# Kernel tuning notes

Measured on AMD Instinct MI355X. Metric: run time of the kernel, lower is better.

The kernel has to match this reference:

```python
import jax, jax.numpy as jnp
import numpy as np

N_NODES = 100000
N_EDGES = 1000000
D_FEAT = 64
N_FILTER = 64
N_CLASSES = 16


def gcn_norm(edge_idx, n):
    """Add self-loops and compute symmetric normalization D^-1/2 (A+I) D^-1/2."""
    loop = jnp.arange(n, dtype=edge_idx.dtype)
    src = jnp.concatenate([edge_idx[0], loop])  # [E+N]
    dst = jnp.concatenate([edge_idx[1], loop])  # [E+N]
    w = jnp.ones(src.shape[0], dtype=jnp.float32)
    deg = jax.ops.segment_sum(w, dst, num_segments=n)  # in-degree incl. self-loop
    dinv = jnp.where(deg > 0, jax.lax.rsqrt(deg), 0.0)
    norm = dinv[src] * w * dinv[dst]  # [E+N]
    return src, dst, norm


def gcn_conv(x, W, b, src, dst, norm, n):
    h = x @ W                                   # [n, f] dense transform first (f <= d)
    msg = h[src] * norm[:, None]                # gather + scale  [E+N, f]
    out = jax.ops.segment_sum(msg, dst, num_segments=n)  # scatter-add  [n, f]
    return out + b


def setup_inputs() -> dict:
    key = jax.random.key(0)
    k1, k2, k3, k4 = jax.random.split(key, 4)
    X = jax.random.normal(k1, (N_NODES, D_FEAT), dtype=jnp.float32)
    edge_idx = jax.random.randint(k2, (2, N_EDGES), 0, N_NODES, dtype=jnp.int64)
    W1 = jax.random.normal(k3, (D_FEAT, N_FILTER), dtype=jnp.float32) * 0.05
    b1 = jnp.zeros((N_FILTER,), dtype=jnp.float32)
    W2 = jax.random.normal(k4, (N_FILTER, N_CLASSES), dtype=jnp.float32) * 0.05
    b2 = jnp.zeros((N_CLASSES,), dtype=jnp.float32)
    return {"X": X, "edge_idx": edge_idx, "W1": W1, "b1": b1, "W2": W2, "b2": b2}


def reference(X, edge_idx, W1, b1, W2, b2):
    n = X.shape[0]
    src, dst, norm = gcn_norm(edge_idx, n)
    x = gcn_conv(X, W1, b1, src, dst, norm, n)
    x = jax.nn.relu(x)
    # dropout p=0 -> identity
    x = gcn_conv(x, W2, b2, src, dst, norm, n)
    return x  # raw logits; pred_layer is not applied in the torch forward
```

## Files before the change

kernel.cpp:

```cpp
#include <hip/hip_runtime.h>
#include <hip/hip_bf16.h>


constexpr int N = 100000;
constexpr int E = 1000000;
constexpr int NB = (N + 511) / 512;
constexpr int CAP = 6144;
constexpr int CSTRIDE = 32;
constexpr int CHUNK = 2048;
constexpr int NBLK = (E + CHUNK - 1) / CHUNK;
constexpr int BT = 512;
constexpr int NPW = 4;
constexpr int NW = (N + NPW - 1) / NPW;
constexpr int NWBLK = (NW + 3) / 4;

__device__ __forceinline__ float bflo(unsigned u) { return __uint_as_float(u << 16); }
__device__ __forceinline__ float bfhi(unsigned u) { return __uint_as_float(u & 0xffff0000u); }

__device__ __forceinline__ void wait_lgkm0() {
    __builtin_amdgcn_s_waitcnt(0xc07f);
    __builtin_amdgcn_sched_barrier(0);
}

__global__ void k_bfill(const int* __restrict__ src, const int* __restrict__ dst,
                        int* __restrict__ cursor, int* __restrict__ bkt) {
    __shared__ int hist[256];
    __shared__ int lbase[256];
    __shared__ int gbase[256];
    __shared__ int lcur[256];
    __shared__ int ws[8];
    __shared__ int stage[CHUNK];
    __shared__ unsigned char sbkt[CHUNK];
    int t = threadIdx.x;
    int lane = t & 63;
    int e0 = blockIdx.x * CHUNK;
    int cnt = min(CHUNK, E - e0);

    if (t < 256) hist[t] = 0;
    __syncthreads();
    for (int j = t; j < cnt; j += BT)
        atomicAdd(&hist[dst[e0 + j] >> 9], 1);
    __syncthreads();
    int h = (t < 256) ? hist[t] : 0;
    int v = h;
#pragma unroll
    for (int off = 1; off < 64; off <<= 1) {
        int u = __shfl_up(v, off);
        if (lane >= off) v += u;
    }
    if (lane == 63) ws[t >> 6] = v;
    __syncthreads();
    int add = 0;
    for (int i = 0; i < (t >> 6); ++i) add += ws[i];
    int inc = v + add;
    if (t < 256) { lbase[t] = inc - h; lcur[t] = 0; }
    if (t < NB) gbase[t] = h ? atomicAdd(&cursor[t * CSTRIDE], h) : 0;
    __syncthreads();
    for (int j = t; j < cnt; j += BT) {
        int d = dst[e0 + j];
        int b = d >> 9;
        int pos = lbase[b] + atomicAdd(&lcur[b], 1);
        stage[pos] = ((d & 511) << 17) | src[e0 + j];
        sbkt[pos] = (unsigned char)b;
    }
    __syncthreads();
    for (int j = t; j < cnt; j += BT) {
        int b = sbkt[j];
        int gpos = gbase[b] + (j - lbase[b]);
        if (gpos < CAP) bkt[b * CAP + gpos] = stage[j];
    }
}

__global__ void k_bfine(const int* __restrict__ cursor, const int* __restrict__ bkt,
                        int* __restrict__ row_ptr, float* __restrict__ dinv,
                        int* __restrict__ csr_src) {
    __shared__ int cnt[512];
    __shared__ int excl[512];
    __shared__ int ws[8];
    int b = blockIdx.x;
    int t = threadIdx.x;
    int lane = t & 63;
    int c = (t < NB) ? cursor[t * CSTRIDE] : 0;
    int mv = (t < b) ? c : 0;
#pragma unroll
    for (int off = 1; off < 64; off <<= 1) mv += __shfl_xor(mv, off);
    if (lane == 0) ws[t >> 6] = mv;
    cnt[t] = 0;
    __syncthreads();
    int base = ws[0] + ws[1] + ws[2] + ws[3] + ws[4] + ws[5] + ws[6] + ws[7];
    int m = cursor[b * CSTRIDE];
    if (b == 0 && t == 0) row_ptr[N] = E;
    const int* bb = bkt + b * CAP;
    const int4* bb4 = (const int4*)bb;
    int m4 = m >> 2;
    for (int j = t; j < m4; j += BT) {
        int4 v = bb4[j];
        atomicAdd(&cnt[v.x >> 17], 1); atomicAdd(&cnt[v.y >> 17], 1);
        atomicAdd(&cnt[v.z >> 17], 1); atomicAdd(&cnt[v.w >> 17], 1);
    }
    for (int j = (m4 << 2) + t; j < m; j += BT) atomicAdd(&cnt[bb[j] >> 17], 1);
    __syncthreads();
    int h = cnt[t];
    int v = h;
#pragma unroll
    for (int off = 1; off < 64; off <<= 1) {
        int u = __shfl_up(v, off);
        if (lane >= off) v += u;
    }
    if (lane == 63) ws[t >> 6] = v;
    __syncthreads();
    int add = 0;
    for (int i = 0; i < (t >> 6); ++i) add += ws[i];
    int ex = v + add - h;
    excl[t] = ex;
    int node = b * 512 + t;
    if (node < N) {
        row_ptr[node] = base + ex;
        dinv[node] = rsqrtf((float)(h + 1));
    }
    __syncthreads();
    for (int j = t; j < m4; j += BT) {
        int4 v4 = bb4[j];
        int p0 = atomicAdd(&excl[v4.x >> 17], 1); csr_src[base + p0] = v4.x & 0x1FFFF;
        int p1 = atomicAdd(&excl[v4.y >> 17], 1); csr_src[base + p1] = v4.y & 0x1FFFF;
        int p2 = atomicAdd(&excl[v4.z >> 17], 1); csr_src[base + p2] = v4.z & 0x1FFFF;
        int p3 = atomicAdd(&excl[v4.w >> 17], 1); csr_src[base + p3] = v4.w & 0x1FFFF;
    }
    for (int j = (m4 << 2) + t; j < m; j += BT) {
        int vv = bb[j];
        int p = atomicAdd(&excl[vv >> 17], 1);
        csr_src[base + p] = vv & 0x1FFFF;
    }
}

__global__ void k_gemm1(const float* __restrict__ X, const float* __restrict__ W1,
                        const float* __restrict__ dinv, __hip_bfloat16* __restrict__ h1s,
                        __hip_bfloat16* __restrict__ h2s) {
    __shared__ float sX[4][4][64];
    int t = threadIdx.x;
    int lane = t & 63;
    int w = t >> 6;
    int wid = (blockIdx.x * 256 + t) >> 6;
    if (blockIdx.x == 0) {
        if (t < 64) h1s[(size_t)N * 64 + t] = __float2bfloat16(0.f);
        if (t < 16) h2s[(size_t)N * 16 + t] = __float2bfloat16(0.f);
    }
    float w1[64];
#pragma unroll
    for (int k = 0; k < 64; ++k) w1[k] = W1[k * 64 + lane];
    constexpr int STRIDE = 4096 * 4;
    int r4 = wid * 4;
    float x0 = X[(size_t)r4 * 64 + lane];
    float x1 = X[(size_t)(r4 + 1) * 64 + lane];
    float x2 = X[(size_t)(r4 + 2) * 64 + lane];
    float x3 = X[(size_t)(r4 + 3) * 64 + lane];
    for (; r4 < N; r4 += STRIDE) {
        int rn = r4 + STRIDE;
        float y0 = 0.f, y1 = 0.f, y2 = 0.f, y3 = 0.f;
        if (rn < N) {
            y0 = X[(size_t)rn * 64 + lane];
            y1 = X[(size_t)(rn + 1) * 64 + lane];
            y2 = X[(size_t)(rn + 2) * 64 + lane];
            y3 = X[(size_t)(rn + 3) * 64 + lane];
        }
        float dv0 = dinv[r4], dv1 = dinv[r4 + 1], dv2 = dinv[r4 + 2], dv3 = dinv[r4 + 3];
        sX[w][0][lane] = x0; sX[w][1][lane] = x1;
        sX[w][2][lane] = x2; sX[w][3][lane] = x3;
        wait_lgkm0();
        float acc0 = 0.f, acc1 = 0.f, acc2 = 0.f, acc3 = 0.f;
#pragma unroll
        for (int k = 0; k < 64; ++k) {
            float wk = w1[k];
            acc0 = fmaf(sX[w][0][k], wk, acc0);
            acc1 = fmaf(sX[w][1][k], wk, acc1);
            acc2 = fmaf(sX[w][2][k], wk, acc2);
            acc3 = fmaf(sX[w][3][k], wk, acc3);
        }
        acc0 *= dv0; acc1 *= dv1; acc2 *= dv2; acc3 *= dv3;
        float up0 = __shfl_xor(acc0, 1);
        float up1 = __shfl_xor(acc1, 1);
        float up2 = __shfl_xor(acc2, 1);
        float up3 = __shfl_xor(acc3, 1);
        if (!(lane & 1)) {
            __hip_bfloat162 p;
            p.x = __float2bfloat16(acc0); p.y = __float2bfloat16(up0);
            *(__hip_bfloat162*)(h1s + (size_t)r4 * 64 + lane) = p;
            p.x = __float2bfloat16(acc1); p.y = __float2bfloat16(up1);
            *(__hip_bfloat162*)(h1s + (size_t)(r4 + 1) * 64 + lane) = p;
            p.x = __float2bfloat16(acc2); p.y = __float2bfloat16(up2);
            *(__hip_bfloat162*)(h1s + (size_t)(r4 + 2) * 64 + lane) = p;
            p.x = __float2bfloat16(acc3); p.y = __float2bfloat16(up3);
            *(__hip_bfloat162*)(h1s + (size_t)(r4 + 3) * 64 + lane) = p;
        }
        x0 = y0; x1 = y1; x2 = y2; x3 = y3;
    }
}

__global__ void k_layer12(const int* __restrict__ row_ptr, const int* __restrict__ csr_src,
                          const float* __restrict__ dinv, const __hip_bfloat16* __restrict__ h1s,
                          const float* __restrict__ b1, const float* __restrict__ W2,
                          __hip_bfloat16* __restrict__ h2s) {
    __shared__ float sy[4][8][72];
    int t = threadIdx.x;
    int lane = t & 63;
    int w = t >> 6;
    int g8 = lane >> 3;
    int qo = (lane & 7) << 4;
    int g16 = lane >> 4, c16 = lane & 15;
    int wid = blockIdx.x * 4 + w;
    int d0 = wid * NPW;
    if (d0 >= N) return;
    int dend = min(d0 + NPW, N);
    float w2[16];
#pragma unroll
    for (int j = 0; j < 16; ++j) w2[j] = W2[(g16 * 16 + j) * 16 + c16];
    float b1v = b1[lane];
    const char* Hb = (const char*)h1s;

    int rp0 = row_ptr[d0];
    for (int d = d0; d < dend; ++d) {
        int rp1 = row_ptr[d + 1];
        float dv = dinv[d];
        float a[8] = {0, 0, 0, 0, 0, 0, 0, 0};
        if (g8 == 0) {
            uint4 u = *(const uint4*)(Hb + (((unsigned)d << 7) | qo));
            a[0] = bflo(u.x); a[1] = bfhi(u.x); a[2] = bflo(u.y); a[3] = bfhi(u.y);
            a[4] = bflo(u.z); a[5] = bfhi(u.z); a[6] = bflo(u.w); a[7] = bfhi(u.w);
        }
        for (int base = rp0; base < rp1; base += 64) {
            int nloc = min(64, rp1 - base);
            int sidx = (lane < nloc) ? csr_src[base + lane] : N;
            int steps = (nloc + 15) >> 4;
            for (int j = 0; j < steps; ++j) {
                int b0 = (j << 4) | g8;
                int s0 = __shfl(sidx, b0);
                int s1 = __shfl(sidx, b0 | 8);
                uint4 u0 = *(const uint4*)(Hb + (((unsigned)s0 << 7) | qo));
                uint4 u1 = *(const uint4*)(Hb + (((unsigned)s1 << 7) | qo));
                a[0] += bflo(u0.x); a[1] += bfhi(u0.x); a[2] += bflo(u0.y); a[3] += bfhi(u0.y);
                a[4] += bflo(u0.z); a[5] += bfhi(u0.z); a[6] += bflo(u0.w); a[7] += bfhi(u0.w);
                a[0] += bflo(u1.x); a[1] += bfhi(u1.x); a[2] += bflo(u1.y); a[3] += bfhi(u1.y);
                a[4] += bflo(u1.z); a[5] += bfhi(u1.z); a[6] += bflo(u1.w); a[7] += bfhi(u1.w);
            }
        }
        rp0 = rp1;
        float* row = &sy[w][g8][(lane & 7) << 3];
        *(float4*)row = make_float4(a[0], a[1], a[2], a[3]);
        *(float4*)(row + 4) = make_float4(a[4], a[5], a[6], a[7]);
        wait_lgkm0();
        float ysum = sy[w][0][lane] + sy[w][1][lane] + sy[w][2][lane] + sy[w][3][lane]
                   + sy[w][4][lane] + sy[w][5][lane] + sy[w][6][lane] + sy[w][7][lane];
        float y = fmaxf(fmaf(dv, ysum, b1v), 0.f);
        float o = 0.f;
#pragma unroll
        for (int j = 0; j < 16; ++j) o = fmaf(__shfl(y, (lane & 48) | j), w2[j], o);
        o += __shfl_xor(o, 16);
        o += __shfl_xor(o, 32);
        o *= dv;
        float oup = __shfl_xor(o, 1);
        if (lane < 16 && !(lane & 1)) {
            __hip_bfloat162 p;
            p.x = __float2bfloat16(o);
            p.y = __float2bfloat16(oup);
            *(__hip_bfloat162*)(h2s + (size_t)d * 16 + lane) = p;
        }
    }
}

__global__ void k_gather2(const int* __restrict__ row_ptr, const int* __restrict__ csr_src,
                          const float* __restrict__ dinv, const __hip_bfloat16* __restrict__ h2s,
                          const float* __restrict__ b2, float* __restrict__ out) {
    int t = threadIdx.x;
    int lane = t & 63;
    int g4 = lane >> 2;
    int q2 = lane & 3;
    int qo = q2 << 3;
    int wid = blockIdx.x * 4 + (t >> 6);
    int d0 = wid * NPW;
    if (d0 >= N) return;
    int dend = min(d0 + NPW, N);
    float b2v[4];
#pragma unroll
    for (int k = 0; k < 4; ++k) b2v[k] = b2[q2 * 4 + k];
    const char* Hb = (const char*)h2s;

    int rp0 = row_ptr[d0];
    for (int d = d0; d < dend; ++d) {
        int rp1 = row_ptr[d + 1];
        float dv = dinv[d];
        float a[4] = {0, 0, 0, 0};
        if (g4 == 0) {
            uint2 u = *(const uint2*)(Hb + (((unsigned)d << 5) | qo));
            a[0] = bflo(u.x); a[1] = bfhi(u.x); a[2] = bflo(u.y); a[3] = bfhi(u.y);
        }
        for (int base = rp0; base < rp1; base += 64) {
            int nloc = min(64, rp1 - base);
            int sidx = (lane < nloc) ? csr_src[base + lane] : N;
            int steps = (nloc + 15) >> 4;
            for (int j = 0; j < steps; ++j) {
                int s = __shfl(sidx, (j << 4) | g4);
                uint2 u = *(const uint2*)(Hb + (((unsigned)s << 5) | qo));
                a[0] += bflo(u.x); a[1] += bfhi(u.x);
                a[2] += bflo(u.y); a[3] += bfhi(u.y);
            }
        }
        rp0 = rp1;
#pragma unroll
        for (int k = 0; k < 4; ++k) {
            a[k] += __shfl_xor(a[k], 4);
            a[k] += __shfl_xor(a[k], 8);
            a[k] += __shfl_xor(a[k], 16);
            a[k] += __shfl_xor(a[k], 32);
        }
        if (lane < 4) {
            float4 r;
            r.x = fmaf(dv, a[0], b2v[0]);
            r.y = fmaf(dv, a[1], b2v[1]);
            r.z = fmaf(dv, a[2], b2v[2]);
            r.w = fmaf(dv, a[3], b2v[3]);
            *(float4*)(out + (size_t)d * 16 + q2 * 4) = r;
        }
    }
}

extern "C" void kernel_launch(void* const* d_in, const int* in_sizes, int n_in,
                              void* d_out, int out_size, void* d_ws, size_t ws_size,
                              hipStream_t stream) {
    const float* X  = (const float*)d_in[0];
    const int*   ei = (const int*)d_in[1];
    const float* W1 = (const float*)d_in[2];
    const float* b1 = (const float*)d_in[3];
    const float* W2 = (const float*)d_in[4];
    const float* b2 = (const float*)d_in[5];
    float* out = (float*)d_out;

    int* cursor  = (int*)d_ws;
    int* row_ptr = cursor + NB * CSTRIDE;
    int* bkt     = row_ptr + N + 4;
    int* csr_src = bkt + NB * CAP;
    float* dinv  = (float*)(csr_src + E);
    __hip_bfloat16* h1s = (__hip_bfloat16*)(dinv + N);
    __hip_bfloat16* h2s = h1s + (size_t)(N + 1) * 64;

    const int* src = ei;
    const int* dst = ei + E;

    hipMemsetAsync(cursor, 0, NB * CSTRIDE * sizeof(int), stream);
    k_bfill<<<NBLK, BT, 0, stream>>>(src, dst, cursor, bkt);
    k_bfine<<<NB, BT, 0, stream>>>(cursor, bkt, row_ptr, dinv, csr_src);
    k_gemm1<<<1024, 256, 0, stream>>>(X, W1, dinv, h1s, h2s);
    k_layer12<<<NWBLK, 256, 0, stream>>>(row_ptr, csr_src, dinv, h1s, b1, W2, h2s);
    k_gather2<<<NWBLK, 256, 0, stream>>>(row_ptr, csr_src, dinv, h2s, b2, out);
}
```

Before: 181.3 us.

## Overlap X@W1 GEMM with bucket fill in one kernel, defer dinv scaling

The first-layer dense transform moves out of its own kernel and into interleaved blocks of the bucket-fill kernel. That lets the GEMM run alongside the edge bucketing instead of after the CSR build. Since dinv is not known yet at that point, the GEMM writes an unscaled fp32 intermediate. k_bfine then scales it by the per-node rsqrt degree and converts it to bf16. This removes one kernel launch and the serial dependency on dinv, but adds an fp32 round trip of the 100k×64 features and raises shared memory use in the fill kernel, which may lower its occupancy.

After: 196.2 us. +8.2%, slower.

```diff
diff --git a/kernel.cpp b/kernel.cpp
--- a/kernel.cpp
+++ b/kernel.cpp
@@ -9,6 +9,8 @@
 constexpr int CSTRIDE = 32;
 constexpr int CHUNK = 2048;
 constexpr int NBLK = (E + CHUNK - 1) / CHUNK;
+constexpr int GB = 512;
+constexpr int FBLK = NBLK + GB;
 constexpr int BT = 512;
 constexpr int NPW = 4;
 constexpr int NW = (N + NPW - 1) / NPW;
@@ -22,8 +24,11 @@
     __builtin_amdgcn_sched_barrier(0);
 }
 
-__global__ void k_bfill(const int* __restrict__ src, const int* __restrict__ dst,
-                        int* __restrict__ cursor, int* __restrict__ bkt) {
+__global__ void k_build(const int* __restrict__ src, const int* __restrict__ dst,
+                        int* __restrict__ cursor, int* __restrict__ bkt,
+                        const float* __restrict__ X, const float* __restrict__ W1,
+                        float* __restrict__ h1u, __hip_bfloat16* __restrict__ h1s,
+                        __hip_bfloat16* __restrict__ h2s) {
     __shared__ int hist[256];
     __shared__ int lbase[256];
     __shared__ int gbase[256];
@@ -31,9 +36,49 @@
     __shared__ int ws[8];
     __shared__ int stage[CHUNK];
     __shared__ unsigned char sbkt[CHUNK];
+    __shared__ float sW[64 * 64];
+    __shared__ float sXg[8][4][64];
+    int bid = blockIdx.x;
     int t = threadIdx.x;
     int lane = t & 63;
-    int e0 = blockIdx.x * CHUNK;
+    bool isfill = (bid < 2 * NBLK) && ((bid & 1) == 0);
+
+    if (!isfill) {
+        int gb = (bid < 2 * NBLK) ? (bid >> 1) : (bid - NBLK);
+        for (int j = t; j < 4096; j += BT) sW[j] = W1[j];
+        if (gb == 0) {
+            if (t < 64) h1s[(size_t)N * 64 + t] = __float2bfloat16(0.f);
+            if (t < 16) h2s[(size_t)N * 16 + t] = __float2bfloat16(0.f);
+        }
+        __syncthreads();
+        int wv = t >> 6;
+        int wid = gb * 8 + wv;
+        for (int r4 = wid * 4; r4 < N; r4 += 4096 * 4) {
+            float x0 = X[(size_t)r4 * 64 + lane];
+            float x1 = X[(size_t)(r4 + 1) * 64 + lane];
+            float x2 = X[(size_t)(r4 + 2) * 64 + lane];
+            float x3 = X[(size_t)(r4 + 3) * 64 + lane];
+            sXg[wv][0][lane] = x0; sXg[wv][1][lane] = x1;
+            sXg[wv][2][lane] = x2; sXg[wv][3][lane] = x3;
+            wait_lgkm0();
+            float acc0 = 0.f, acc1 = 0.f, acc2 = 0.f, acc3 = 0.f;
+#pragma unroll
+            for (int k = 0; k < 64; ++k) {
+                float wk = sW[k * 64 + lane];
+                acc0 = fmaf(sXg[wv][0][k], wk, acc0);
+                acc1 = fmaf(sXg[wv][1][k], wk, acc1);
+                acc2 = fmaf(sXg[wv][2][k], wk, acc2);
+                acc3 = fmaf(sXg[wv][3][k], wk, acc3);
+            }
+            h1u[(size_t)r4 * 64 + lane] = acc0;
+            h1u[(size_t)(r4 + 1) * 64 + lane] = acc1;
+            h1u[(size_t)(r4 + 2) * 64 + lane] = acc2;
+            h1u[(size_t)(r4 + 3) * 64 + lane] = acc3;
+        }
+        return;
+    }
+    int fb = bid >> 1;
+    int e0 = fb * CHUNK;
     int cnt = min(CHUNK, E - e0);
 
     if (t < 256) hist[t] = 0;
@@ -73,7 +118,8 @@
 
 __global__ void k_bfine(const int* __restrict__ cursor, const int* __restrict__ bkt,
                         int* __restrict__ row_ptr, float* __restrict__ dinv,
-                        int* __restrict__ csr_src) {
+                        int* __restrict__ csr_src,
+                        const float* __restrict__ h1u, __hip_bfloat16* __restrict__ h1s) {
     __shared__ int cnt[512];
     __shared__ int excl[512];
     __shared__ int ws[8];
@@ -131,68 +177,18 @@
         int p = atomicAdd(&excl[vv >> 17], 1);
         csr_src[base + p] = vv & 0x1FFFF;
     }
-}
-
-__global__ void k_gemm1(const float* __restrict__ X, const float* __restrict__ W1,
-                        const float* __restrict__ dinv, __hip_bfloat16* __restrict__ h1s,
-                        __hip_bfloat16* __restrict__ h2s) {
-    __shared__ float sX[4][4][64];
-    int t = threadIdx.x;
-    int lane = t & 63;
-    int w = t >> 6;
-    int wid = (blockIdx.x * 256 + t) >> 6;
-    if (blockIdx.x == 0) {
-        if (t < 64) h1s[(size_t)N * 64 + t] = __float2bfloat16(0.f);
-        if (t < 16) h2s[(size_t)N * 16 + t] = __float2bfloat16(0.f);
-    }
-    float w1[64];
-#pragma unroll
-    for (int k = 0; k < 64; ++k) w1[k] = W1[k * 64 + lane];
-    constexpr int STRIDE = 4096 * 4;
-    int r4 = wid * 4;
-    float x0 = X[(size_t)r4 * 64 + lane];
-    float x1 = X[(size_t)(r4 + 1) * 64 + lane];
-    float x2 = X[(size_t)(r4 + 2) * 64 + lane];
-    float x3 = X[(size_t)(r4 + 3) * 64 + lane];
-    for (; r4 < N; r4 += STRIDE) {
-        int rn = r4 + STRIDE;
-        float y0 = 0.f, y1 = 0.f, y2 = 0.f, y3 = 0.f;
-        if (rn < N) {
-            y0 = X[(size_t)rn * 64 + lane];
-            y1 = X[(size_t)(rn + 1) * 64 + lane];
-            y2 = X[(size_t)(rn + 2) * 64 + lane];
-            y3 = X[(size_t)(rn + 3) * 64 + lane];
-        }
-        float dv0 = dinv[r4], dv1 = dinv[r4 + 1], dv2 = dinv[r4 + 2], dv3 = dinv[r4 + 3];
-        sX[w][0][lane] = x0; sX[w][1][lane] = x1;
-        sX[w][2][lane] = x2; sX[w][3][lane] = x3;
-        wait_lgkm0();
-        float acc0 = 0.f, acc1 = 0.f, acc2 = 0.f, acc3 = 0.f;
-#pragma unroll
-        for (int k = 0; k < 64; ++k) {
-            float wk = w1[k];
-            acc0 = fmaf(sX[w][0][k], wk, acc0);
-            acc1 = fmaf(sX[w][1][k], wk, acc1);
-            acc2 = fmaf(sX[w][2][k], wk, acc2);
-            acc3 = fmaf(sX[w][3][k], wk, acc3);
-        }
-        acc0 *= dv0; acc1 *= dv1; acc2 *= dv2; acc3 *= dv3;
-        float up0 = __shfl_xor(acc0, 1);
-        float up1 = __shfl_xor(acc1, 1);
-        float up2 = __shfl_xor(acc2, 1);
-        float up3 = __shfl_xor(acc3, 1);
-        if (!(lane & 1)) {
-            __hip_bfloat162 p;
-            p.x = __float2bfloat16(acc0); p.y = __float2bfloat16(up0);
-            *(__hip_bfloat162*)(h1s + (size_t)r4 * 64 + lane) = p;
-            p.x = __float2bfloat16(acc1); p.y = __float2bfloat16(up1);
-            *(__hip_bfloat162*)(h1s + (size_t)(r4 + 1) * 64 + lane) = p;
-            p.x = __float2bfloat16(acc2); p.y = __float2bfloat16(up2);
-            *(__hip_bfloat162*)(h1s + (size_t)(r4 + 2) * 64 + lane) = p;
-            p.x = __float2bfloat16(acc3); p.y = __float2bfloat16(up3);
-            *(__hip_bfloat162*)(h1s + (size_t)(r4 + 3) * 64 + lane) = p;
-        }
-        x0 = y0; x1 = y1; x2 = y2; x3 = y3;
+    for (int j = t; j < 512 * 16; j += BT) {
+        int r = j >> 4, ch = j & 15;
+        int nd = b * 512 + r;
+        if (nd < N) {
+            float sd = rsqrtf((float)(cnt[r] + 1));
+            float4 vv = *(const float4*)(h1u + (size_t)nd * 64 + ch * 4);
+            __hip_bfloat162 p0, p1;
+            p0.x = __float2bfloat16(vv.x * sd); p0.y = __float2bfloat16(vv.y * sd);
+            p1.x = __float2bfloat16(vv.z * sd); p1.y = __float2bfloat16(vv.w * sd);
+            __hip_bfloat162* dst2 = (__hip_bfloat162*)(h1s + (size_t)nd * 64 + ch * 4);
+            dst2[0] = p0; dst2[1] = p1;
+        }
     }
 }
 
@@ -339,16 +335,16 @@
     int* bkt     = row_ptr + N + 4;
     int* csr_src = bkt + NB * CAP;
     float* dinv  = (float*)(csr_src + E);
-    __hip_bfloat16* h1s = (__hip_bfloat16*)(dinv + N);
+    float* h1u   = dinv + N;
+    __hip_bfloat16* h1s = (__hip_bfloat16*)(h1u + (size_t)(N + 1) * 64);
     __hip_bfloat16* h2s = h1s + (size_t)(N + 1) * 64;
 
     const int* src = ei;
     const int* dst = ei + E;
 
     hipMemsetAsync(cursor, 0, NB * CSTRIDE * sizeof(int), stream);
-    k_bfill<<<NBLK, BT, 0, stream>>>(src, dst, cursor, bkt);
-    k_bfine<<<NB, BT, 0, stream>>>(cursor, bkt, row_ptr, dinv, csr_src);
-    k_gemm1<<<1024, 256, 0, stream>>>(X, W1, dinv, h1s, h2s);
+    k_build<<<FBLK, BT, 0, stream>>>(src, dst, cursor, bkt, X, W1, h1u, h1s, h2s);
+    k_bfine<<<NB, BT, 0, stream>>>(cursor, bkt, row_ptr, dinv, csr_src, h1u, h1s);
     k_layer12<<<NWBLK, 256, 0, stream>>>(row_ptr, csr_src, dinv, h1s, b1, W2, h2s);
     k_gather2<<<NWBLK, 256, 0, stream>>>(row_ptr, csr_src, dinv, h2s, b2, out);
 }
```
